# Kernel tuning notes

Hardware: AMD Instinct MI355X
Metric: run time of the kernel (lower is better)

The kernel has to match this reference:

```python
import jax, jax.numpy as jnp
import numpy as np

B, N, E, H = 2, 1000, 2000, 128


def setup_inputs() -> dict:
    key = jax.random.key(0)
    k1, k2, k3, k4, k5 = jax.random.split(key, 5)
    node_state = jax.random.normal(k1, (B, N, H), dtype=jnp.float32)
    edge_vec = jax.random.normal(k2, (B, E, H), dtype=jnp.float32)
    node2edge = jax.random.uniform(k3, (B, E, N), dtype=jnp.float32)
    edge2node = jax.random.uniform(k4, (B, N, E), dtype=jnp.float32)
    # xavier_uniform for a (H, H, H) tensor: fan_in = H*H, fan_out = H (torch views last 2 dims)
    bound = float(np.sqrt(6.0 / (H + H * H)))
    edge_network = jax.random.uniform(k5, (H, H, H), dtype=jnp.float32, minval=-bound, maxval=bound)
    return {
        "node_state": node_state,
        "edge_vec": edge_vec,
        "node2edge": node2edge,
        "edge2node": edge2node,
        "edge_network": edge_network,
    }


def reference(node_state, edge_vec, node2edge, edge2node, edge_network):
    # node2edge_emb[b,e,h] = sum_n node2edge[b,e,n] * node_state[b,n,h]
    n2e_emb = jnp.einsum("ben,bnh->beh", node2edge, node_state)
    # per-edge dynamic weight W[b,e,i,j] = sum_h edge_vec[b,e,h] * edge_network[h,i,j],
    # applied to n2e_emb; fused into one contraction (grouped edge-conditioned conv).
    new_n2e = jnp.einsum("beh,hij,bej->bei", edge_vec, edge_network, n2e_emb)
    norm = jnp.sum(edge2node, axis=2, keepdims=True) + 1.0  # [B,N,1]
    agg = (jnp.einsum("bne,bei->bni", edge2node, new_n2e) + node_state) / norm
    return agg
```

## Files before the change

### kernel.cpp

```cpp
#include <hip/hip_runtime.h>
#include <hip/hip_bf16.h>
#include <stdint.h>

#define Bv 2
#define Nv 1000
#define Ev 2000
#define Hv 128

typedef __attribute__((ext_vector_type(8))) short bf16x8;
typedef __attribute__((ext_vector_type(4))) float f32x4;
typedef unsigned short u16;
typedef unsigned int u32;

static __device__ __forceinline__ u32 pack2bf(float a, float b) {
  union { __hip_bfloat162 h; u32 u; } c;
  c.h = __float22bfloat162_rn(make_float2(a, b));
  return c.u;
}
static __device__ __forceinline__ u16 cvt1bf(float a) {
  return (u16)(pack2bf(a, 0.f) & 0xffffu);
}

static __device__ __forceinline__ void gload_lds16(const void* g, void* l) {
  __builtin_amdgcn_global_load_lds(
      (const __attribute__((address_space(1))) void*)g,
      (__attribute__((address_space(3))) void*)l, 16, 0, 0);
}

__global__ void k_prep_ns(const float* __restrict__ ns, u16* __restrict__ nsT) {
  __shared__ float tile[32][33];
  const int bid = blockIdx.x;
  const int t = threadIdx.x;
  const int x = bid & 31, y = (bid >> 5) & 3, z = bid >> 7;
  const float* src = ns + (size_t)z * Nv * Hv;
  u16* dst = nsT + (size_t)z * Hv * 1024;
  const int r0 = x * 32, c0 = y * 32;
  const int tx = t & 31, ty = t >> 5;
#pragma unroll
  for (int rr = 0; rr < 4; ++rr) {
    int r = r0 + ty + rr * 8;
    int c = c0 + tx;
    float v = (r < Nv) ? src[(size_t)r * Hv + c] : 0.f;
    tile[ty + rr * 8][tx] = v;
  }
  __syncthreads();
#pragma unroll
  for (int rr = 0; rr < 4; ++rr) {
    int oc = c0 + ty + rr * 8;
    int orr = r0 + tx;
    dst[(size_t)oc * 1024 + orr] = cvt1bf(tile[tx][ty + rr * 8]);
  }
}

template <int M, int KREAL, int KPAD, int NKC, int KSTEPS, int NMT, bool ROWSUM, bool FCVT>
__launch_bounds__(256, 4)
__global__ void k_gemm_flat(const float* __restrict__ A, const u16* __restrict__ BT,
                            float* __restrict__ Cpart, float* __restrict__ nrmpart,
                            const float* __restrict__ en, u16* __restrict__ enbf) {
  __shared__ u16 AL[64 * 136];
  __shared__ float rowsum[64];
  const int id = blockIdx.x;
  const int t = threadIdx.x;
  if (FCVT && id >= NKC * NMT * 2) {
    const int cb = id - NKC * NMT * 2;
    size_t idx = ((size_t)cb * 256u + t) * 8u;
    const f32x4* p = (const f32x4*)(en + idx);
    f32x4 a = p[0], b = p[1];
    uint4 o;
    o.x = pack2bf(a.x, a.y);
    o.y = pack2bf(a.z, a.w);
    o.z = pack2bf(b.x, b.y);
    o.w = pack2bf(b.z, b.w);
    *(uint4*)(enbf + idx) = o;
    return;
  }
  const int kcid = id % NKC;
  const int mt = (id / NKC) % NMT;
  const int b = id / (NKC * NMT);
  A     += (size_t)b * M * KREAL;
  BT    += (size_t)b * 128 * KPAD;
  Cpart += (size_t)kcid * (2 * M * 128) + (size_t)b * M * 128;
  if (ROWSUM) nrmpart += (size_t)kcid * (2 * M) + (size_t)b * M;
  const int lane = t & 63;
  const int w = t >> 6;
  const int row16 = lane & 15;
  const int kg = lane >> 4;
  const int mrow0 = mt * 64;
  const int mtg = (w >> 1) * 2;
  const int itg = (w & 1) * 4;
  f32x4 acc[2][4];
#pragma unroll
  for (int i = 0; i < 2; ++i)
#pragma unroll
    for (int j = 0; j < 4; ++j) acc[i][j] = (f32x4){0.f, 0.f, 0.f, 0.f};
  if (ROWSUM && t < 64) rowsum[t] = 0.f;

#pragma unroll 1
  for (int s = 0; s < KSTEPS; ++s) {
    const int kc = (kcid * KSTEPS + s) * 128;
    __syncthreads();
#pragma unroll
    for (int r = 0; r < 4; ++r) {
      const int chunk = t + r * 256;
      const int m = chunk >> 4;
      const int jc = (chunk & 15) * 8;
      const int gm = mrow0 + m;
      const int gk = kc + jc;
      f32x4 x0 = {0.f, 0.f, 0.f, 0.f}, x1 = {0.f, 0.f, 0.f, 0.f};
      if (gm < M && gk + 8 <= KREAL) {
        const f32x4* p = (const f32x4*)(A + (size_t)gm * KREAL + gk);
        x0 = p[0];
        x1 = p[1];
      }
      if (ROWSUM) {
        float s8 = x0.x + x0.y + x0.z + x0.w + x1.x + x1.y + x1.z + x1.w;
        s8 += __shfl_down(s8, 8, 16);
        s8 += __shfl_down(s8, 4, 16);
        s8 += __shfl_down(s8, 2, 16);
        s8 += __shfl_down(s8, 1, 16);
        if ((lane & 15) == 0) rowsum[m] += s8;
      }
      uint4 o;
      o.x = pack2bf(x0.x, x0.y);
      o.y = pack2bf(x0.z, x0.w);
      o.z = pack2bf(x1.x, x1.y);
      o.w = pack2bf(x1.z, x1.w);
      *(uint4*)&AL[m * 136 + jc] = o;
    }
    __syncthreads();
#pragma unroll
    for (int kk = 0; kk < 4; ++kk) {
      bf16x8 a[2], bfr[4];
#pragma unroll
      for (int q = 0; q < 2; ++q)
        a[q] = *(const bf16x8*)&AL[((mtg + q) * 16 + row16) * 136 + kk * 32 + kg * 8];
#pragma unroll
      for (int q = 0; q < 4; ++q)
        bfr[q] = *(const bf16x8*)(BT + (size_t)((itg + q) * 16 + row16) * KPAD + kc + kk * 32 + kg * 8);
#pragma unroll
      for (int mi = 0; mi < 2; ++mi)
#pragma unroll
        for (int ii = 0; ii < 4; ++ii)
          acc[mi][ii] = __builtin_amdgcn_mfma_f32_16x16x32_bf16(a[mi], bfr[ii], acc[mi][ii], 0, 0, 0);
    }
  }
  if (ROWSUM && t < 64 && mrow0 + t < M) nrmpart[mrow0 + t] = rowsum[t];
#pragma unroll
  for (int mi = 0; mi < 2; ++mi) {
#pragma unroll
    for (int r = 0; r < 4; ++r) {
      const int lrow = (mtg + mi) * 16 + kg * 4 + r;
      const int gm = mrow0 + lrow;
      if (gm < M) {
#pragma unroll
        for (int ii = 0; ii < 4; ++ii)
          Cpart[(size_t)gm * 128 + (itg + ii) * 16 + row16] = acc[mi][ii][r];
      }
    }
  }
}

__global__ void k_cvt_red(const u16* __restrict__ part2, u16* __restrict__ neweT) {
  const int tid = blockIdx.x * 256 + threadIdx.x;
  const size_t f0 = (size_t)tid * 8;
  const int m0 = (int)(f0 & 2047);
  uint4 o;
  if (m0 >= Ev) {
    o = make_uint4(0, 0, 0, 0);
  } else {
    float s[8] = {0.f, 0.f, 0.f, 0.f, 0.f, 0.f, 0.f, 0.f};
#pragma unroll
    for (int hg = 0; hg < 8; ++hg) {
      uint4 v = *(const uint4*)(part2 + (size_t)hg * 524288 + f0);
      u32 wv[4] = {v.x, v.y, v.z, v.w};
#pragma unroll
      for (int q = 0; q < 4; ++q) {
        s[2 * q]     += __uint_as_float(wv[q] << 16);
        s[2 * q + 1] += __uint_as_float(wv[q] & 0xffff0000u);
      }
    }
    o.x = pack2bf(s[0], s[1]);
    o.y = pack2bf(s[2], s[3]);
    o.z = pack2bf(s[4], s[5]);
    o.w = pack2bf(s[6], s[7]);
  }
  *(uint4*)(neweT + f0) = o;
}

__global__ void k_epi_red(const float* __restrict__ part3, const float* __restrict__ nrmp,
                          const float* __restrict__ ns, float* __restrict__ out) {
  const int tid = blockIdx.x * 256 + threadIdx.x;
  const size_t f0 = (size_t)tid * 4;
  const int row = (int)(f0 >> 7);
  const f32x4* p = (const f32x4*)(part3 + f0);
  f32x4 s = {0.f, 0.f, 0.f, 0.f};
#pragma unroll
  for (int kc = 0; kc < 8; ++kc) s += p[(size_t)kc * 64000];
  float nm = 1.0f;
#pragma unroll
  for (int kc = 0; kc < 8; ++kc) nm += nrmp[(size_t)kc * 2000 + row];
  f32x4 nsv = *(const f32x4*)(ns + f0);
  *(f32x4*)(out + f0) = (s + nsv) * (1.0f / nm);
}

__launch_bounds__(256, 2)
__global__ void k_edge_mix(const float* __restrict__ ev, const float* __restrict__ part1,
                           const u16* __restrict__ enbf, u16* __restrict__ part2) {
  __shared__ u16 APL[4][4096];
  __shared__ u16 U[64 * 136];
  __shared__ float EVL[64 * 20];
  const int id = blockIdx.x;
  const int hgrp = id & 7;
  const int rest = id >> 3;
  const int mt = rest & 31;
  const int b = rest >> 5;
  const int h0 = hgrp * 16;
  const int t = threadIdx.x;
  const int lane = t & 63;
  const int w = t >> 6;
  const int row16 = lane & 15;
  const int kg = lane >> 4;
  const int mbase = mt * 64;

  {
    const float* pb = part1 + (size_t)b * 256000 + (size_t)mbase * 128;
#pragma unroll
    for (int r = 0; r < 8; ++r) {
      const int chunk = t + r * 256;
      const int row = chunk >> 5;
      const int c4 = (chunk & 31) * 4;
      const int gm = mbase + row;
      f32x4 s = {0.f, 0.f, 0.f, 0.f};
      if (gm < Ev) {
        const float* p = pb + (size_t)row * 128 + c4;
#pragma unroll
        for (int kc = 0; kc < 4; ++kc) s += *(const f32x4*)(p + (size_t)kc * 512000);
      }
      *(uint2*)&U[row * 136 + c4] = make_uint2(pack2bf(s.x, s.y), pack2bf(s.z, s.w));
    }
  }

  if (t < 64) {
    const int ml = mbase + t;
    const float* src = ev + ((size_t)b * Ev + ml) * Hv + h0;
    const f32x4 z = {0.f, 0.f, 0.f, 0.f};
#pragma unroll
    for (int q = 0; q < 4; ++q) {
      f32x4 v = (ml < Ev) ? *(const f32x4*)(src + q * 4) : z;
      *(f32x4*)&EVL[t * 20 + q * 4] = v;
    }
  }

  auto STAGE = [&](int h) {
    const char* plane = (const char*)(enbf + (size_t)h * 16384) + (size_t)w * 8192;
    char* dst = (char*)&APL[w][0];
#pragma unroll
    for (int it = 0; it < 8; ++it) {
      const int r = it * 4 + (lane >> 4);
      const int inner = (lane & 15) << 4;
      const int srcb = r * 256 + (inner ^ ((r & 7) << 4));
      gload_lds16(plane + srcb, dst + it * 1024);
    }
  };

  STAGE(h0);
  __syncthreads();

  bf16x8 bfrag[4][4];
#pragma unroll
  for (int mf = 0; mf < 4; ++mf)
#pragma unroll
    for (int kk = 0; kk < 4; ++kk)
      bfrag[mf][kk] = *(const bf16x8*)&U[(mf * 16 + row16) * 136 + kk * 32 + kg * 8];

  const f32x4 zero4 = {0.f, 0.f, 0.f, 0.f};
  f32x4 pers[2][4];
#pragma unroll
  for (int fi = 0; fi < 2; ++fi)
#pragma unroll
    for (int mf = 0; mf < 4; ++mf) pers[fi][mf] = zero4;

  const int xorv = (row16 & 7) << 4;

#pragma unroll 1
  for (int hh = 0; hh < 16; ++hh) {
    asm volatile("s_waitcnt vmcnt(0)" ::: "memory");
    __builtin_amdgcn_sched_barrier(0);
    const char* sl = (const char*)&APL[w][0];
    bf16x8 a[2][4];
#pragma unroll
    for (int fi = 0; fi < 2; ++fi) {
      const int rs = fi * 16 + row16;
#pragma unroll
      for (int kk = 0; kk < 4; ++kk)
        a[fi][kk] = *(const bf16x8*)(sl + rs * 256 + ((kk * 64 + kg * 16) ^ xorv));
    }
    if (hh + 1 < 16) {
      asm volatile("s_waitcnt lgkmcnt(0)" ::: "memory");
      __builtin_amdgcn_sched_barrier(0);
      STAGE(h0 + hh + 1);
    }
    f32x4 q[2][4];
#pragma unroll
    for (int fi = 0; fi < 2; ++fi)
#pragma unroll
      for (int mf = 0; mf < 4; ++mf)
        q[fi][mf] = __builtin_amdgcn_mfma_f32_16x16x32_bf16(a[fi][0], bfrag[mf][0], zero4, 0, 0, 0);
#pragma unroll
    for (int kk = 1; kk < 4; ++kk)
#pragma unroll
      for (int fi = 0; fi < 2; ++fi)
#pragma unroll
        for (int mf = 0; mf < 4; ++mf)
          q[fi][mf] = __builtin_amdgcn_mfma_f32_16x16x32_bf16(a[fi][kk], bfrag[mf][kk], q[fi][mf], 0, 0, 0);
    float evv[4];
#pragma unroll
    for (int mf = 0; mf < 4; ++mf)
      evv[mf] = EVL[(mf * 16 + row16) * 20 + hh];
#pragma unroll
    for (int fi = 0; fi < 2; ++fi)
#pragma unroll
      for (int mf = 0; mf < 4; ++mf)
        pers[fi][mf] += evv[mf] * q[fi][mf];
  }

  u16* slice = part2 + (size_t)hgrp * (2 * 128 * 2048);
#pragma unroll
  for (int fi = 0; fi < 2; ++fi) {
#pragma unroll
    for (int mf = 0; mf < 4; ++mf) {
      const int ml = mbase + mf * 16 + row16;
#pragma unroll
      for (int r = 0; r < 4; ++r) {
        const int irow = w * 32 + fi * 16 + kg * 4 + r;
        slice[((size_t)b * 128 + irow) * 2048 + ml] = cvt1bf(pers[fi][mf][r]);
      }
    }
  }
}

extern "C" void kernel_launch(void* const* d_in, const int* in_sizes, int n_in,
                              void* d_out, int out_size, void* d_ws, size_t ws_size,
                              hipStream_t stream) {
  const float* ns  = (const float*)d_in[0];
  const float* ev  = (const float*)d_in[1];
  const float* n2e = (const float*)d_in[2];
  const float* e2n = (const float*)d_in[3];
  const float* en  = (const float*)d_in[4];
  float* out = (float*)d_out;

  char* ws = (char*)d_ws;
  float* part1 = (float*)(ws);
  u16*   part2 = (u16*)  (ws + 8192000);
  float* part3 = (float*)(ws + 16580608);
  float* nrmp  = (float*)(ws + 24772608);
  u16*   enbf  = (u16*)  (ws + 24838144);
  u16*   nsT   = (u16*)  (ws + 29032448);
  u16*   neweT = (u16*)  (ws + 29556736);

  k_prep_ns<<<dim3(256), dim3(256), 0, stream>>>(ns, nsT);
  k_gemm_flat<2000, 1000, 1024, 4, 2, 32, false, true>
      <<<dim3(1280), dim3(256), 0, stream>>>(n2e, nsT, part1, nullptr, en, enbf);
  k_edge_mix<<<dim3(512), dim3(256), 0, stream>>>(ev, part1, enbf, part2);
  k_cvt_red<<<dim3(256), dim3(256), 0, stream>>>(part2, neweT);
  k_gemm_flat<1000, 2000, 2048, 8, 2, 16, true, false>
      <<<dim3(256), dim3(256), 0, stream>>>(e2n, neweT, part3, nrmp, nullptr, nullptr);
  k_epi_red<<<dim3(250), dim3(256), 0, stream>>>(part3, nrmp, ns, out);
}
```

Before: 65.22 us.

## Fuse split-K reductions into producer kernels via last-block atomic counters

Split-K partial sums are now reduced inside the producing kernels. The last block to finish each tile, detected with an atomic counter and thread fences, does the reduction, so the standalone k_cvt_red and k_epi_red kernels and their launches go away. The first GEMM also writes a reduced bf16 embedding that edge_mix loads straight into registers, instead of every edge_mix block re-reducing the fp32 partials into LDS. This adds counter zeroing in the prep kernel and serial tail work in the last-arriving blocks.

Result: slower. 232.8 us (+257.0%).

```diff
diff --git a/kernel.cpp b/kernel.cpp
--- a/kernel.cpp
+++ b/kernel.cpp
@@ -27,10 +27,12 @@
       (__attribute__((address_space(3))) void*)l, 16, 0, 0);
 }
 
-__global__ void k_prep_ns(const float* __restrict__ ns, u16* __restrict__ nsT) {
+__global__ void k_prep_ns(const float* __restrict__ ns, u16* __restrict__ nsT,
+                          int* __restrict__ cnts) {
   __shared__ float tile[32][33];
   const int bid = blockIdx.x;
   const int t = threadIdx.x;
+  if (bid == 0 && t < 160) cnts[t] = 0;
   const int x = bid & 31, y = (bid >> 5) & 3, z = bid >> 7;
   const float* src = ns + (size_t)z * Nv * Hv;
   u16* dst = nsT + (size_t)z * Hv * 1024;
@@ -52,17 +54,15 @@
   }
 }
 
-template <int M, int KREAL, int KPAD, int NKC, int KSTEPS, int NMT, bool ROWSUM, bool FCVT>
 __launch_bounds__(256, 4)
-__global__ void k_gemm_flat(const float* __restrict__ A, const u16* __restrict__ BT,
-                            float* __restrict__ Cpart, float* __restrict__ nrmpart,
-                            const float* __restrict__ en, u16* __restrict__ enbf) {
-  __shared__ u16 AL[64 * 136];
-  __shared__ float rowsum[64];
+__global__ void k_gemm1(const float* __restrict__ A, const u16* __restrict__ BT,
+                        float* __restrict__ part1, u16* __restrict__ embbf,
+                        const float* __restrict__ en, u16* __restrict__ enbf,
+                        int* __restrict__ cnt) {
   const int id = blockIdx.x;
   const int t = threadIdx.x;
-  if (FCVT && id >= NKC * NMT * 2) {
-    const int cb = id - NKC * NMT * 2;
+  if (id >= 256) {
+    const int cb = id - 256;
     size_t idx = ((size_t)cb * 256u + t) * 8u;
     const f32x4* p = (const f32x4*)(en + idx);
     f32x4 a = p[0], b = p[1];
@@ -74,13 +74,14 @@
     *(uint4*)(enbf + idx) = o;
     return;
   }
-  const int kcid = id % NKC;
-  const int mt = (id / NKC) % NMT;
-  const int b = id / (NKC * NMT);
-  A     += (size_t)b * M * KREAL;
-  BT    += (size_t)b * 128 * KPAD;
-  Cpart += (size_t)kcid * (2 * M * 128) + (size_t)b * M * 128;
-  if (ROWSUM) nrmpart += (size_t)kcid * (2 * M) + (size_t)b * M;
+  __shared__ u16 AL[64 * 136];
+  __shared__ int lastf;
+  const int kcid = id & 3;
+  const int mt = (id >> 2) & 31;
+  const int b = id >> 7;
+  const float* Ab = A + (size_t)b * 2000 * 1000;
+  const u16* BTb = BT + (size_t)b * 128 * 1024;
+  float* Cpart = part1 + (size_t)kcid * 512000 + (size_t)b * 256000;
   const int lane = t & 63;
   const int w = t >> 6;
   const int row16 = lane & 15;
@@ -93,11 +94,10 @@
   for (int i = 0; i < 2; ++i)
 #pragma unroll
     for (int j = 0; j < 4; ++j) acc[i][j] = (f32x4){0.f, 0.f, 0.f, 0.f};
-  if (ROWSUM && t < 64) rowsum[t] = 0.f;
 
 #pragma unroll 1
-  for (int s = 0; s < KSTEPS; ++s) {
-    const int kc = (kcid * KSTEPS + s) * 128;
+  for (int s = 0; s < 2; ++s) {
+    const int kc = (kcid * 2 + s) * 128;
     __syncthreads();
 #pragma unroll
     for (int r = 0; r < 4; ++r) {
@@ -107,18 +107,10 @@
       const int gm = mrow0 + m;
       const int gk = kc + jc;
       f32x4 x0 = {0.f, 0.f, 0.f, 0.f}, x1 = {0.f, 0.f, 0.f, 0.f};
-      if (gm < M && gk + 8 <= KREAL) {
-        const f32x4* p = (const f32x4*)(A + (size_t)gm * KREAL + gk);
+      if (gm < 2000 && gk + 8 <= 1000) {
+        const f32x4* p = (const f32x4*)(Ab + (size_t)gm * 1000 + gk);
         x0 = p[0];
         x1 = p[1];
-      }
-      if (ROWSUM) {
-        float s8 = x0.x + x0.y + x0.z + x0.w + x1.x + x1.y + x1.z + x1.w;
-        s8 += __shfl_down(s8, 8, 16);
-        s8 += __shfl_down(s8, 4, 16);
-        s8 += __shfl_down(s8, 2, 16);
-        s8 += __shfl_down(s8, 1, 16);
-        if ((lane & 15) == 0) rowsum[m] += s8;
       }
       uint4 o;
       o.x = pack2bf(x0.x, x0.y);
@@ -136,7 +128,7 @@
         a[q] = *(const bf16x8*)&AL[((mtg + q) * 16 + row16) * 136 + kk * 32 + kg * 8];
 #pragma unroll
       for (int q = 0; q < 4; ++q)
-        bfr[q] = *(const bf16x8*)(BT + (size_t)((itg + q) * 16 + row16) * KPAD + kc + kk * 32 + kg * 8);
+        bfr[q] = *(const bf16x8*)(BTb + (size_t)((itg + q) * 16 + row16) * 1024 + kc + kk * 32 + kg * 8);
 #pragma unroll
       for (int mi = 0; mi < 2; ++mi)
 #pragma unroll
@@ -144,71 +136,49 @@
           acc[mi][ii] = __builtin_amdgcn_mfma_f32_16x16x32_bf16(a[mi], bfr[ii], acc[mi][ii], 0, 0, 0);
     }
   }
-  if (ROWSUM && t < 64 && mrow0 + t < M) nrmpart[mrow0 + t] = rowsum[t];
 #pragma unroll
   for (int mi = 0; mi < 2; ++mi) {
 #pragma unroll
     for (int r = 0; r < 4; ++r) {
       const int lrow = (mtg + mi) * 16 + kg * 4 + r;
       const int gm = mrow0 + lrow;
-      if (gm < M) {
+      if (gm < 2000) {
 #pragma unroll
         for (int ii = 0; ii < 4; ++ii)
           Cpart[(size_t)gm * 128 + (itg + ii) * 16 + row16] = acc[mi][ii][r];
       }
     }
   }
-}
-
-__global__ void k_cvt_red(const u16* __restrict__ part2, u16* __restrict__ neweT) {
-  const int tid = blockIdx.x * 256 + threadIdx.x;
-  const size_t f0 = (size_t)tid * 8;
-  const int m0 = (int)(f0 & 2047);
-  uint4 o;
-  if (m0 >= Ev) {
-    o = make_uint4(0, 0, 0, 0);
-  } else {
-    float s[8] = {0.f, 0.f, 0.f, 0.f, 0.f, 0.f, 0.f, 0.f};
-#pragma unroll
-    for (int hg = 0; hg < 8; ++hg) {
-      uint4 v = *(const uint4*)(part2 + (size_t)hg * 524288 + f0);
-      u32 wv[4] = {v.x, v.y, v.z, v.w};
-#pragma unroll
-      for (int q = 0; q < 4; ++q) {
-        s[2 * q]     += __uint_as_float(wv[q] << 16);
-        s[2 * q + 1] += __uint_as_float(wv[q] & 0xffff0000u);
-      }
-    }
-    o.x = pack2bf(s[0], s[1]);
-    o.y = pack2bf(s[2], s[3]);
-    o.z = pack2bf(s[4], s[5]);
-    o.w = pack2bf(s[6], s[7]);
-  }
-  *(uint4*)(neweT + f0) = o;
-}
-
-__global__ void k_epi_red(const float* __restrict__ part3, const float* __restrict__ nrmp,
-                          const float* __restrict__ ns, float* __restrict__ out) {
-  const int tid = blockIdx.x * 256 + threadIdx.x;
-  const size_t f0 = (size_t)tid * 4;
-  const int row = (int)(f0 >> 7);
-  const f32x4* p = (const f32x4*)(part3 + f0);
-  f32x4 s = {0.f, 0.f, 0.f, 0.f};
-#pragma unroll
-  for (int kc = 0; kc < 8; ++kc) s += p[(size_t)kc * 64000];
-  float nm = 1.0f;
-#pragma unroll
-  for (int kc = 0; kc < 8; ++kc) nm += nrmp[(size_t)kc * 2000 + row];
-  f32x4 nsv = *(const f32x4*)(ns + f0);
-  *(f32x4*)(out + f0) = (s + nsv) * (1.0f / nm);
+  __threadfence();
+  __syncthreads();
+  if (t == 0) lastf = (atomicAdd(&cnt[b * 32 + mt], 1) == 3) ? 1 : 0;
+  __syncthreads();
+  if (!lastf) return;
+  __threadfence();
+  const float* pb = part1 + (size_t)b * 256000 + (size_t)mrow0 * 128;
+  u16* eb = embbf + ((size_t)b * 2048 + mrow0) * 128;
+#pragma unroll
+  for (int c = 0; c < 8; ++c) {
+    const int idx2 = t + c * 256;
+    const int r = idx2 >> 5, c4 = (idx2 & 31) * 4;
+    const int gm = mrow0 + r;
+    f32x4 s = {0.f, 0.f, 0.f, 0.f};
+    if (gm < 2000) {
+      const float* p = pb + (size_t)r * 128 + c4;
+#pragma unroll
+      for (int kc = 0; kc < 4; ++kc) s += *(const f32x4*)(p + (size_t)kc * 512000);
+    }
+    *(uint2*)(eb + (size_t)r * 128 + c4) = make_uint2(pack2bf(s.x, s.y), pack2bf(s.z, s.w));
+  }
 }
 
 __launch_bounds__(256, 2)
-__global__ void k_edge_mix(const float* __restrict__ ev, const float* __restrict__ part1,
-                           const u16* __restrict__ enbf, u16* __restrict__ part2) {
+__global__ void k_edge_mix(const float* __restrict__ ev, const u16* __restrict__ embbf,
+                           const u16* __restrict__ enbf, u16* __restrict__ part2,
+                           u16* __restrict__ neweT, int* __restrict__ cnt) {
   __shared__ u16 APL[4][4096];
-  __shared__ u16 U[64 * 136];
   __shared__ float EVL[64 * 20];
+  __shared__ int lastf;
   const int id = blockIdx.x;
   const int hgrp = id & 7;
   const int rest = id >> 3;
@@ -222,24 +192,6 @@
   const int kg = lane >> 4;
   const int mbase = mt * 64;
 
-  {
-    const float* pb = part1 + (size_t)b * 256000 + (size_t)mbase * 128;
-#pragma unroll
-    for (int r = 0; r < 8; ++r) {
-      const int chunk = t + r * 256;
-      const int row = chunk >> 5;
-      const int c4 = (chunk & 31) * 4;
-      const int gm = mbase + row;
-      f32x4 s = {0.f, 0.f, 0.f, 0.f};
-      if (gm < Ev) {
-        const float* p = pb + (size_t)row * 128 + c4;
-#pragma unroll
-        for (int kc = 0; kc < 4; ++kc) s += *(const f32x4*)(p + (size_t)kc * 512000);
-      }
-      *(uint2*)&U[row * 136 + c4] = make_uint2(pack2bf(s.x, s.y), pack2bf(s.z, s.w));
-    }
-  }
-
   if (t < 64) {
     const int ml = mbase + t;
     const float* src = ev + ((size_t)b * Ev + ml) * Hv + h0;
@@ -248,6 +200,18 @@
     for (int q = 0; q < 4; ++q) {
       f32x4 v = (ml < Ev) ? *(const f32x4*)(src + q * 4) : z;
       *(f32x4*)&EVL[t * 20 + q * 4] = v;
+    }
+  }
+
+  bf16x8 bfrag[4][4];
+  {
+    const u16* ebase = embbf + ((size_t)b * 2048 + mbase) * 128;
+#pragma unroll
+    for (int mf = 0; mf < 4; ++mf) {
+      const u16* rp = ebase + (size_t)(mf * 16 + row16) * 128;
+#pragma unroll
+      for (int kk = 0; kk < 4; ++kk)
+        bfrag[mf][kk] = *(const bf16x8*)(rp + kk * 32 + kg * 8);
     }
   }
 
@@ -263,16 +227,6 @@
     }
   };
 
-  STAGE(h0);
-  __syncthreads();
-
-  bf16x8 bfrag[4][4];
-#pragma unroll
-  for (int mf = 0; mf < 4; ++mf)
-#pragma unroll
-    for (int kk = 0; kk < 4; ++kk)
-      bfrag[mf][kk] = *(const bf16x8*)&U[(mf * 16 + row16) * 136 + kk * 32 + kg * 8];
-
   const f32x4 zero4 = {0.f, 0.f, 0.f, 0.f};
   f32x4 pers[2][4];
 #pragma unroll
@@ -281,6 +235,9 @@
     for (int mf = 0; mf < 4; ++mf) pers[fi][mf] = zero4;
 
   const int xorv = (row16 & 7) << 4;
+
+  STAGE(h0);
+  __syncthreads();
 
 #pragma unroll 1
   for (int hh = 0; hh < 16; ++hh) {
@@ -335,6 +292,154 @@
         const int irow = w * 32 + fi * 16 + kg * 4 + r;
         slice[((size_t)b * 128 + irow) * 2048 + ml] = cvt1bf(pers[fi][mf][r]);
       }
+    }
+  }
+  __threadfence();
+  __syncthreads();
+  if (t == 0) lastf = (atomicAdd(&cnt[b * 32 + mt], 1) == 7) ? 1 : 0;
+  __syncthreads();
+  if (!lastf) return;
+  __threadfence();
+#pragma unroll
+  for (int c = 0; c < 4; ++c) {
+    const int idx2 = t + c * 256;
+    const int i = idx2 >> 3, mo = (idx2 & 7) * 8;
+    const size_t off = ((size_t)b * 128 + i) * 2048 + mbase + mo;
+    float s[8] = {0.f, 0.f, 0.f, 0.f, 0.f, 0.f, 0.f, 0.f};
+#pragma unroll
+    for (int hg = 0; hg < 8; ++hg) {
+      uint4 v = *(const uint4*)(part2 + (size_t)hg * 524288 + off);
+      u32 wv[4] = {v.x, v.y, v.z, v.w};
+#pragma unroll
+      for (int q = 0; q < 4; ++q) {
+        s[2 * q]     += __uint_as_float(wv[q] << 16);
+        s[2 * q + 1] += __uint_as_float(wv[q] & 0xffff0000u);
+      }
+    }
+    uint4 o;
+    o.x = pack2bf(s[0], s[1]);
+    o.y = pack2bf(s[2], s[3]);
+    o.z = pack2bf(s[4], s[5]);
+    o.w = pack2bf(s[6], s[7]);
+    *(uint4*)(neweT + off) = o;
+  }
+}
+
+__launch_bounds__(256, 4)
+__global__ void k_gemm2(const float* __restrict__ A, const u16* __restrict__ BT,
+                        float* __restrict__ part3, float* __restrict__ nrmp,
+                        const float* __restrict__ ns, float* __restrict__ out,
+                        int* __restrict__ cnt) {
+  __shared__ u16 AL[64 * 136];
+  __shared__ float rowsum[64];
+  __shared__ int lastf;
+  const int id = blockIdx.x;
+  const int t = threadIdx.x;
+  const int kcid = id & 7;
+  const int mt = (id >> 3) & 15;
+  const int b = id >> 7;
+  const float* Ab = A + (size_t)b * 1000 * 2000;
+  const u16* BTb = BT + (size_t)b * 128 * 2048;
+  float* Cpart = part3 + (size_t)kcid * 256000 + (size_t)b * 128000;
+  float* nrmb = nrmp + (size_t)kcid * 2000 + (size_t)b * 1000;
+  const int lane = t & 63;
+  const int w = t >> 6;
+  const int row16 = lane & 15;
+  const int kg = lane >> 4;
+  const int mrow0 = mt * 64;
+  const int mtg = (w >> 1) * 2;
+  const int itg = (w & 1) * 4;
+  f32x4 acc[2][4];
+#pragma unroll
+  for (int i = 0; i < 2; ++i)
+#pragma unroll
+    for (int j = 0; j < 4; ++j) acc[i][j] = (f32x4){0.f, 0.f, 0.f, 0.f};
+  if (t < 64) rowsum[t] = 0.f;
+
+#pragma unroll 1
+  for (int s = 0; s < 2; ++s) {
+    const int kc = (kcid * 2 + s) * 128;
+    __syncthreads();
+#pragma unroll
+    for (int r = 0; r < 4; ++r) {
+      const int chunk = t + r * 256;
+      const int m = chunk >> 4;
+      const int jc = (chunk & 15) * 8;
+      const int gm = mrow0 + m;
+      const int gk = kc + jc;
+      f32x4 x0 = {0.f, 0.f, 0.f, 0.f}, x1 = {0.f, 0.f, 0.f, 0.f};
+      if (gm < 1000 && gk + 8 <= 2000) {
+        const f32x4* p = (const f32x4*)(Ab + (size_t)gm * 2000 + gk);
+        x0 = p[0];
+        x1 = p[1];
+      }
+      float s8 = x0.x + x0.y + x0.z + x0.w + x1.x + x1.y + x1.z + x1.w;
+      s8 += __shfl_down(s8, 8, 16);
+      s8 += __shfl_down(s8, 4, 16);
+      s8 += __shfl_down(s8, 2, 16);
+      s8 += __shfl_down(s8, 1, 16);
+      if ((lane & 15) == 0) rowsum[m] += s8;
+      uint4 o;
+      o.x = pack2bf(x0.x, x0.y);
+      o.y = pack2bf(x0.z, x0.w);
+      o.z = pack2bf(x1.x, x1.y);
+      o.w = pack2bf(x1.z, x1.w);
+      *(uint4*)&AL[m * 136 + jc] = o;
+    }
+    __syncthreads();
+#pragma unroll
+    for (int kk = 0; kk < 4; ++kk) {
+      bf16x8 a[2], bfr[4];
+#pragma unroll
+      for (int q = 0; q < 2; ++q)
+        a[q] = *(const bf16x8*)&AL[((mtg + q) * 16 + row16) * 136 + kk * 32 + kg * 8];
+#pragma unroll
+      for (int q = 0; q < 4; ++q)
+        bfr[q] = *(const bf16x8*)(BTb + (size_t)((itg + q) * 16 + row16) * 2048 + kc + kk * 32 + kg * 8);
+#pragma unroll
+      for (int mi = 0; mi < 2; ++mi)
+#pragma unroll
+        for (int ii = 0; ii < 4; ++ii)
+          acc[mi][ii] = __builtin_amdgcn_mfma_f32_16x16x32_bf16(a[mi], bfr[ii], acc[mi][ii], 0, 0, 0);
+    }
+  }
+  if (t < 64 && mrow0 + t < 1000) nrmb[mrow0 + t] = rowsum[t];
+#pragma unroll
+  for (int mi = 0; mi < 2; ++mi) {
+#pragma unroll
+    for (int r = 0; r < 4; ++r) {
+      const int lrow = (mtg + mi) * 16 + kg * 4 + r;
+      const int gm = mrow0 + lrow;
+      if (gm < 1000) {
+#pragma unroll
+        for (int ii = 0; ii < 4; ++ii)
+          Cpart[(size_t)gm * 128 + (itg + ii) * 16 + row16] = acc[mi][ii][r];
+      }
+    }
+  }
+  __threadfence();
+  __syncthreads();
+  if (t == 0) lastf = (atomicAdd(&cnt[b * 16 + mt], 1) == 7) ? 1 : 0;
+  __syncthreads();
+  if (!lastf) return;
+  __threadfence();
+  const float* pb = part3 + (size_t)b * 128000 + (size_t)mrow0 * 128;
+#pragma unroll
+  for (int c = 0; c < 8; ++c) {
+    const int idx2 = t + c * 256;
+    const int r = idx2 >> 5, c4 = (idx2 & 31) * 4;
+    const int gm = mrow0 + r;
+    if (gm < 1000) {
+      const float* p = pb + (size_t)r * 128 + c4;
+      f32x4 s = {0.f, 0.f, 0.f, 0.f};
+#pragma unroll
+      for (int kc = 0; kc < 8; ++kc) s += *(const f32x4*)(p + (size_t)kc * 256000);
+      float nm = 1.0f;
+#pragma unroll
+      for (int kc = 0; kc < 8; ++kc) nm += nrmp[(size_t)kc * 2000 + b * 1000 + gm];
+      const size_t o = ((size_t)b * 1000 + gm) * 128 + c4;
+      f32x4 nsv = *(const f32x4*)(ns + o);
+      *(f32x4*)(out + o) = (s + nsv) * (1.0f / nm);
     }
   }
 }
@@ -354,16 +459,14 @@
   u16*   part2 = (u16*)  (ws + 8192000);
   float* part3 = (float*)(ws + 16580608);
   float* nrmp  = (float*)(ws + 24772608);
-  u16*   enbf  = (u16*)  (ws + 24838144);
-  u16*   nsT   = (u16*)  (ws + 29032448);
-  u16*   neweT = (u16*)  (ws + 29556736);
-
-  k_prep_ns<<<dim3(256), dim3(256), 0, stream>>>(ns, nsT);
-  k_gemm_flat<2000, 1000, 1024, 4, 2, 32, false, true>
-      <<<dim3(1280), dim3(256), 0, stream>>>(n2e, nsT, part1, nullptr, en, enbf);
-  k_edge_mix<<<dim3(512), dim3(256), 0, stream>>>(ev, part1, enbf, part2);
-  k_cvt_red<<<dim3(256), dim3(256), 0, stream>>>(part2, neweT);
-  k_gemm_flat<1000, 2000, 2048, 8, 2, 16, true, false>
-      <<<dim3(256), dim3(256), 0, stream>>>(e2n, neweT, part3, nrmp, nullptr, nullptr);
-  k_epi_red<<<dim3(250), dim3(256), 0, stream>>>(part3, nrmp, ns, out);
-}
+  u16*   embbf = (u16*)  (ws + 24838144);
+  u16*   enbf  = (u16*)  (ws + 25886720);
+  u16*   nsT   = (u16*)  (ws + 30081024);
+  u16*   neweT = (u16*)  (ws + 30605312);
+  int*   cnts  = (int*)  (ws + 31653888);
+
+  k_prep_ns<<<dim3(256), dim3(256), 0, stream>>>(ns, nsT, cnts);
+  k_gemm1<<<dim3(1280), dim3(256), 0, stream>>>(n2e, nsT, part1, embbf, en, enbf, cnts);
+  k_edge_mix<<<dim3(512), dim3(256), 0, stream>>>(ev, embbf, enbf, part2, neweT, cnts + 64);
+  k_gemm2<<<dim3(256), dim3(256), 0, stream>>>(e2n, neweT, part3, nrmp, ns, out, cnts + 128);
+}
```
